# Kernel tuning notes

Measured on AMD Instinct MI355X. Metric: run time of the kernel, lower is better.

The kernel has to match this reference:

```python
import jax, jax.numpy as jnp
import numpy as np

N_NODES = 50000
N_EDGES = 800000
GEN_EPS = 1e-7
LN_EPS = 1e-5


def _mlp3_tanh(x, w0, b0, w1, b1, w2, b2):
    x = jnp.tanh(x @ w0.T + b0)
    x = jnp.tanh(x @ w1.T + b1)
    return jnp.tanh(x @ w2.T + b2)


def _gen_conv(x, src, dst, edge_attr, w0, b0, ln_w, ln_b, w1, b1):
    # GENConv(aggr='softmax', t=1): msg = relu(x_j + e) + eps
    msg = jax.nn.relu(x[src] + edge_attr) + GEN_EPS          # [E, 64]
    m = jax.ops.segment_max(msg, dst, num_segments=N_NODES)  # [N, 64]
    ex = jnp.exp(msg - m[dst])
    den = jax.ops.segment_sum(ex, dst, num_segments=N_NODES)
    alpha = ex / den[dst]                                    # scatter-softmax per dst
    agg = jax.ops.segment_sum(alpha * msg, dst, num_segments=N_NODES)
    h = x + agg                                              # x_r + aggregated messages
    # internal MLP: Linear(64->128), LayerNorm(128), ReLU, Linear(128->64)
    h = h @ w0.T + b0
    mu = jnp.mean(h, axis=-1, keepdims=True)
    var = jnp.mean((h - mu) ** 2, axis=-1, keepdims=True)
    h = ln_w * (h - mu) * jax.lax.rsqrt(var + LN_EPS) + ln_b
    h = jax.nn.relu(h)
    return h @ w1.T + b1


def setup_inputs() -> dict:
    key = jax.random.key(0)
    ks = jax.random.split(key, 32)
    s = 0.05
    d = {
        'node_features': jax.random.normal(ks[0], (N_NODES, 11), jnp.float32),
        'edge_features': jax.random.normal(ks[1], (N_EDGES, 3), jnp.float32),
        'edge_index': jax.random.randint(ks[2], (2, N_EDGES), 0, N_NODES, jnp.int32),
        'ne_w0': jax.random.normal(ks[3], (64, 11)) * s, 'ne_b0': jnp.zeros((64,)),
        'ne_w1': jax.random.normal(ks[4], (64, 64)) * s, 'ne_b1': jnp.zeros((64,)),
        'ne_w2': jax.random.normal(ks[5], (64, 64)) * s, 'ne_b2': jnp.zeros((64,)),
        'ee_w0': jax.random.normal(ks[6], (64, 3)) * s, 'ee_b0': jnp.zeros((64,)),
        'ee_w1': jax.random.normal(ks[7], (64, 64)) * s, 'ee_b1': jnp.zeros((64,)),
        'ee_w2': jax.random.normal(ks[8], (64, 64)) * s, 'ee_b2': jnp.zeros((64,)),
        'mp_w0': jax.random.normal(ks[9], (3, 128, 64)) * s,
        'mp_b0': jnp.zeros((3, 128)),
        'mp_ln_w': jnp.ones((3, 128)), 'mp_ln_b': jnp.zeros((3, 128)),
        'mp_w1': jax.random.normal(ks[10], (3, 64, 128)) * s,
        'mp_b1': jnp.zeros((3, 64)),
        'pi_w0': jax.random.normal(ks[11], (64, 64)) * s, 'pi_b0': jnp.zeros((64,)),
        'pi_w1': jax.random.normal(ks[12], (64, 64)) * s, 'pi_b1': jnp.zeros((64,)),
        'pi_w2': jax.random.normal(ks[13], (2, 64)) * s, 'pi_b2': jnp.zeros((2,)),
    }
    return {k: (v.astype(jnp.float32) if v.dtype != jnp.int32 else v) for k, v in d.items()}


def reference(node_features, edge_features, edge_index,
              ne_w0, ne_b0, ne_w1, ne_b1, ne_w2, ne_b2,
              ee_w0, ee_b0, ee_w1, ee_b1, ee_w2, ee_b2,
              mp_w0, mp_b0, mp_ln_w, mp_ln_b, mp_w1, mp_b1,
              pi_w0, pi_b0, pi_w1, pi_b1, pi_w2, pi_b2):
    src, dst = edge_index[0], edge_index[1]
    x = _mlp3_tanh(node_features, ne_w0, ne_b0, ne_w1, ne_b1, ne_w2, ne_b2)
    e = _mlp3_tanh(edge_features, ee_w0, ee_b0, ee_w1, ee_b1, ee_w2, ee_b2)
    for i in range(3):
        x = _gen_conv(x, src, dst, e, mp_w0[i], mp_b0[i], mp_ln_w[i], mp_ln_b[i], mp_w1[i], mp_b1[i])
    h = jnp.tanh(x @ pi_w0.T + pi_b0)
    h = jnp.tanh(h @ pi_w1.T + pi_b1)
    out = h @ pi_w2.T + pi_b2                 # [N, 2]
    # output.t().reshape(-1)[:n_turbines] == first column of out
    means = -30.0 + (out[:, 0] + 1.0) * 60.0 / 2.0
    return means
```

## Files before the change

kernel.cpp:

```cpp
#include <hip/hip_runtime.h>
#include <hip/hip_fp16.h>
#include <stdint.h>

#define N_NODES 50000
#define N_EDGES 800000

typedef unsigned short u16;
typedef unsigned int u32;
typedef __attribute__((ext_vector_type(8))) short short8;
typedef __attribute__((ext_vector_type(4))) float f32x4;
typedef __attribute__((ext_vector_type(4))) u32 u32x4;
typedef __attribute__((ext_vector_type(2))) u32 u32x2;

#define WAVE_SYNC() asm volatile("s_waitcnt lgkmcnt(0)" ::: "memory")

__device__ __forceinline__ float b2f(u16 v) {
    u32 u = ((u32)v) << 16; float f; __builtin_memcpy(&f, &u, 4); return f;
}
__device__ __forceinline__ u16 f2b(float f) {
    u32 u; __builtin_memcpy(&u, &f, 4);
    return (u16)((u + 0x8000u) >> 16);
}
__device__ __forceinline__ float lo2f(u32 p) {
    u32 u = p << 16; float f; __builtin_memcpy(&f, &u, 4); return f;
}
__device__ __forceinline__ float hi2f(u32 p) {
    u32 u = p & 0xffff0000u; float f; __builtin_memcpy(&f, &u, 4); return f;
}
__device__ __forceinline__ u32 pack2(float a, float b) {
    u32 ua, ub; __builtin_memcpy(&ua, &a, 4); __builtin_memcpy(&ub, &b, 4);
    return __builtin_amdgcn_perm(ub + 0x8000u, ua + 0x8000u, 0x07060302u);
}
__device__ __forceinline__ f32x4 mfma16(short8 a, short8 b, f32x4 c) {
    return __builtin_amdgcn_mfma_f32_16x16x32_bf16(a, b, c, 0, 0, 0);
}

__device__ __forceinline__ bool detect_bf(const void* nf) {
    u32 w = ((const u32*)nf)[threadIdx.x & 63];
    u32 lo = w & 0xffffu;
    int e = (int)((lo >> 7) & 0xff);
    int good = ((e >= 118 && e <= 132) || lo == 0) ? 1 : 0;
    unsigned long long b = __ballot(good != 0);
    return __popcll(b) >= 48;
}

#define TANH_TBL_N 256
__device__ __forceinline__ void load_tbl(const u32* __restrict__ g, u32* tbl) {
    int i = (int)threadIdx.x;
    if (i < TANH_TBL_N) tbl[i] = g[i];
    __syncthreads();
}
__device__ __forceinline__ float lut_tanh(const u32* __restrict__ tbl, float x) {
    float a = __builtin_fabsf(x);
    a = fminf(a, 7.96875f);
    int i = (int)(a * 32.f);
    u32 e = tbl[i];
    __half2 h2; __builtin_memcpy(&h2, &e, 4);
    float b = __half2float(__low2half(h2));
    float s = __half2float(__high2half(h2));
    return copysignf(fmaf(s, a, b), x);
}

enum : int {
    NE_B0 = 704,   NE_B1 = 4864,  NE_B2 = 9024,
    EE_B0 = 9280,  EE_B1 = 13440, EE_B2 = 17600,
    MP_B0 = 42240, LNW_O = 42624, LNB_O = 43008, MP_B1 = 67968,
    PI_B0 = 72256, PI_B1 = 76416, PI_W2 = 76480, PI_B2 = 76608,
    W_TOTAL = 76610
};

enum : int {
    FR_EE1 = 0, FR_EE2 = 4, FR_EE3 = 12, FR_NE1 = 20, FR_NE2 = 24, FR_NE3 = 32,
    FR_MP0 = 40, FR_MP1 = 88, FR_PI0 = 136, FR_PI1 = 144, FR_TOTAL = 152
};

#define OFF_W       ((size_t)0)
#define OFF_WB      ((size_t)0x61000)
#define OFF_TBL     ((size_t)0x88000)
#define OFF_XB0     ((size_t)0x90000)
#define OFF_XB1     ((size_t)0x700000)
#define OFF_H64B    ((size_t)0xE00000)
#define OFF_E       ((size_t)0x1500000)
#define OFF_ROWPTR  ((size_t)0x8300000)
#define OFF_CURSOR  ((size_t)0x8340000)
#define OFF_CNT     ((size_t)0x8380000)
#define OFF_PERM    ((size_t)0x83C0000)
#define OFF_SRCS    ((size_t)0x8700000)
#define OFF_BSUM    ((size_t)0x8A80000)

struct Ptrs24 { const void* p[24]; };

#define PREP_FRAG   (FR_TOTAL * 512)
#define PREP_BIAS   (PREP_FRAG + 1986)
#define PREP_LUT    (PREP_BIAS + TANH_TBL_N)
#define PREP_TOTAL  (PREP_LUT + N_NODES)

__global__ void prep_kernel(const void* nf, Ptrs24 ps, float* __restrict__ W,
                            u16* __restrict__ Wb, u32* __restrict__ gtbl,
                            int* __restrict__ cnts) {
    bool bf = detect_bf(nf);
    int t = blockIdx.x * blockDim.x + threadIdx.x;
    if (t < PREP_FRAG) {
        const int base[15] = {FR_EE1,FR_EE2,FR_EE3,FR_NE1,FR_NE2,FR_NE3,
                              FR_MP0,FR_MP0+16,FR_MP0+32, FR_MP1,FR_MP1+16,FR_MP1+32,
                              FR_PI0,FR_PI1,FR_TOTAL};
        const int psrc[14]  = {6,8,10, 0,2,4, 12,12,12, 16,16,16, 18,20};
        const int soff[14]  = {0,0,0, 0,0,0, 0,8192,16384, 0,8192,16384, 0,0};
        const int kreal[14] = {3,64,64, 11,64,64, 64,64,64, 128,128,128, 64,64};
        const int nn[14]    = {64,64,64, 64,64,64, 128,128,128, 64,64,64, 64,64};
        int f = t >> 9, r = t & 511, lane = r >> 3, j = r & 7;
        int l = 0;
        while (f >= base[l + 1]) l++;
        int lf = f - base[l];
        int NT = nn[l] >> 4;
        int kt = lf / NT, nt = lf % NT;
        int k = kt * 32 + (lane >> 4) * 8 + j;
        int n = nt * 16 + (lane & 15);
        float v = 0.f;
        if (k < kreal[l]) {
            long idx = (long)soff[l] + (long)n * kreal[l] + k;
            const void* p = ps.p[psrc[l]];
            v = bf ? b2f(((const u16*)p)[idx]) : ((const float*)p)[idx];
        }
        u32 u; __builtin_memcpy(&u, &v, 4);
        Wb[t] = (u16)((u + 0x7fffu + ((u >> 16) & 1u)) >> 16);
        return;
    }
    if (t < PREP_BIAS) {
        int t2 = t - PREP_FRAG;
        const int cnt[14]  = {64,64,64, 64,64,64, 384,384,384,192, 64,64,128,2};
        const int wdst[14] = {NE_B0,NE_B1,NE_B2, EE_B0,EE_B1,EE_B2,
                              MP_B0,LNW_O,LNB_O,MP_B1, PI_B0,PI_B1,PI_W2,PI_B2};
        const int sp[14]   = {1,3,5, 7,9,11, 13,14,15,17, 19,21,22,23};
        int sgi = 0, off = t2;
        while (off >= cnt[sgi]) { off -= cnt[sgi]; sgi++; }
        const void* p = ps.p[sp[sgi]];
        W[wdst[sgi] + off] = bf ? b2f(((const u16*)p)[off]) : ((const float*)p)[off];
        return;
    }
    if (t < PREP_LUT) {
        int i = t - PREP_BIAS;
        float x0 = i * 0.03125f, x1 = x0 + 0.03125f;
        float t0 = tanhf(x0), t1 = tanhf(x1);
        float s = (t1 - t0) * 32.f;
        float b = fmaf(-s, x0, t0);
        __half hs = __float2half(s), hb = __float2half(b);
        u16 us, ub;
        __builtin_memcpy(&us, &hs, 2); __builtin_memcpy(&ub, &hb, 2);
        gtbl[i] = (u32)ub | ((u32)us << 16);
        return;
    }
    if (t < PREP_TOTAL) cnts[t - PREP_LUT] = 0;
}


__global__ void hist_kernel(const int* __restrict__ dst, int* __restrict__ cnts) {
    int e = blockIdx.x * blockDim.x + threadIdx.x;
    if (e < N_EDGES) atomicAdd(&cnts[dst[e]], 1);
}

__global__ void scanA(const int* __restrict__ cnts, int* __restrict__ prow,
                      int* __restrict__ bsum) {
    __shared__ int wsum[16];
    int tid = threadIdx.x, lane = tid & 63, wid = tid >> 6;
    int i0 = blockIdx.x * 2048 + tid * 2;
    int v0 = 0, v1 = 0;
    if (i0 >= 1 && i0 <= N_NODES) v0 = (cnts[i0 - 1] + 1) & ~1;
    if (i0 + 1 <= N_NODES && i0 + 1 >= 1) v1 = (cnts[i0] + 1) & ~1;
    int v = v0 + v1;
#pragma unroll
    for (int off = 1; off < 64; off <<= 1) {
        int t = __shfl_up(v, off, 64);
        if (lane >= off) v += t;
    }
    if (lane == 63) wsum[wid] = v;
    __syncthreads();
    if (tid == 0) { int a = 0; for (int w = 0; w < 16; w++) { a += wsum[w]; wsum[w] = a; } }
    __syncthreads();
    int incl = v + (wid ? wsum[wid - 1] : 0);
    if (i0 <= N_NODES) prow[i0] = incl - v1;
    if (i0 + 1 <= N_NODES) prow[i0 + 1] = incl;
    if (tid == 1023) bsum[blockIdx.x] = incl;
}
__global__ void scanC(const int* __restrict__ bsum, const int* __restrict__ cnts,
                      int* __restrict__ prow, int* __restrict__ cursor,
                      int* __restrict__ srcs) {
    int i = blockIdx.x * 1024 + threadIdx.x;
    if (i > N_NODES) return;
    int nb = (int)(blockIdx.x >> 1);
    int add = 0;
    for (int b = 0; b < nb; b++) add += bsum[b];
    int v = prow[i] + add;
    prow[i] = v;
    if (i < N_NODES) {
        cursor[i] = v;
        int c = cnts[i];
        if (c & 1) srcs[v + c] = -1;
    }
}

__global__ void scatter_kernel(const int* __restrict__ dst, const int* __restrict__ src,
                               int* __restrict__ cursor, int* __restrict__ perm,
                               int* __restrict__ srcs) {
    int e = blockIdx.x * blockDim.x + threadIdx.x;
    if (e >= N_EDGES) return;
    int p = atomicAdd(&cursor[dst[e]], 1);
    perm[e] = p;
    srcs[p] = src[e];
}


template<int KT, int NT, int INSTR>
__device__ __forceinline__ void mfma_layer(const u32* ldsin, int lane,
        const short8* __restrict__ Wf, int basef, const float* __restrict__ bias, f32x4* acc) {
    int q = lane >> 4, mr = lane & 15;
#pragma unroll
    for (int nt = 0; nt < NT; nt++) acc[nt] = *(const f32x4*)(bias + nt * 16 + q * 4);
#pragma unroll
    for (int kt = 0; kt < KT; kt++) {
        short8 act = *(const short8*)(ldsin + mr * INSTR + kt * 16 + q * 4);
#pragma unroll
        for (int nt = 0; nt < NT; nt++)
            acc[nt] = mfma16(Wf[(basef + kt * NT + nt) * 64 + lane], act, acc[nt]);
    }
}

template<int KT, int NT>
__device__ __forceinline__ void mfma_layer_reg(const short8* act, int lane,
        const short8* __restrict__ Wf, int basef, const float* __restrict__ bias, f32x4* acc) {
    int q = lane >> 4;
#pragma unroll
    for (int nt = 0; nt < NT; nt++) acc[nt] = *(const f32x4*)(bias + nt * 16 + q * 4);
#pragma unroll
    for (int kt = 0; kt < KT; kt++)
#pragma unroll
        for (int nt = 0; nt < NT; nt++)
            acc[nt] = mfma16(Wf[(basef + kt * NT + nt) * 64 + lane], act[kt], acc[nt]);
}

template<int NT, int OUTSTR>
__device__ __forceinline__ void tanh_pack_lds(const f32x4* acc, u32* ldsout, int lane,
                                              const u32* __restrict__ tbl) {
    int q = lane >> 4, mr = lane & 15;
#pragma unroll
    for (int nt = 0; nt < NT; nt++) {
        f32x4 a = acc[nt];
        u32x2 pb;
        pb.x = pack2(lut_tanh(tbl, a[0]), lut_tanh(tbl, a[1]));
        pb.y = pack2(lut_tanh(tbl, a[2]), lut_tanh(tbl, a[3]));
        *(u32x2*)&ldsout[mr * OUTSTR + nt * 8 + q * 2] = pb;
    }
}

__device__ __forceinline__ void zero_stage(u32* B0, int lane) {
#pragma unroll
    for (int it = 0; it < 4; it++) {
        int f = lane + 64 * it;
        B0[(f >> 4) * 36 + (f & 15)] = 0;
    }
}


#define EDGE_SPLIT_BLOCKS (N_EDGES / 128)

__global__ __launch_bounds__(256) void edge_encoder(const void* nf, const void* ef,
        u32* __restrict__ ebuf, const int* __restrict__ perm, const float* __restrict__ W,
        const short8* __restrict__ Wf, const u32* __restrict__ gtbl, int part) {
    __shared__ u32 lds[4 * 1152];
    __shared__ u32 tbl[TANH_TBL_N];
    bool bf = detect_bf(nf);
    load_tbl(gtbl, tbl);
    int wv = threadIdx.x >> 6, lane = threadIdx.x & 63;
    u32* B0 = lds + wv * 1152;
    u32* B1 = B0 + 576;
    long ebase = ((long)blockIdx.x + (long)part * EDGE_SPLIT_BLOCKS) * 64 + wv * 16;
    zero_stage(B0, lane);
    if (lane < 16) {
        long e = ebase + lane;
        float i0, i1, i2;
        if (bf) { const u16* p = (const u16*)ef + e * 3; i0 = b2f(p[0]); i1 = b2f(p[1]); i2 = b2f(p[2]); }
        else    { const float* p = (const float*)ef + e * 3; i0 = p[0]; i1 = p[1]; i2 = p[2]; }
        u32* row = B0 + lane * 36;
        row[0] = pack2(i0, i1); row[1] = pack2(i2, 0.f);
    }
    WAVE_SYNC();
    f32x4 acc[4];
    mfma_layer<1, 4, 36>(B0, lane, Wf, FR_EE1, W + EE_B0, acc);
    tanh_pack_lds<4, 36>(acc, B1, lane, tbl);
    WAVE_SYNC();
    mfma_layer<2, 4, 36>(B1, lane, Wf, FR_EE2, W + EE_B1, acc);
    tanh_pack_lds<4, 36>(acc, B0, lane, tbl);
    WAVE_SYNC();
    mfma_layer<2, 4, 36>(B0, lane, Wf, FR_EE3, W + EE_B2, acc);
    tanh_pack_lds<4, 36>(acc, B1, lane, tbl);
    WAVE_SYNC();
    int ro = lane >> 2, cc = (lane & 3) * 8;
    long e = ebase + ro;
    long prowp = perm[e];
    u32x4 v0 = *(const u32x4*)&B1[ro * 36 + cc];
    u32x4 v1 = *(const u32x4*)&B1[ro * 36 + cc + 4];
    *(u32x4*)&ebuf[prowp * 32 + cc] = v0;
    *(u32x4*)&ebuf[prowp * 32 + cc + 4] = v1;
}

__global__ __launch_bounds__(256) void node_encoder(const void* nf,
        u16* __restrict__ xbf, const float* __restrict__ W,
        const short8* __restrict__ Wf, const u32* __restrict__ gtbl) {
    __shared__ u32 lds[4 * 1152];
    __shared__ u32 tbl[TANH_TBL_N];
    bool bf = detect_bf(nf);
    load_tbl(gtbl, tbl);
    int wv = threadIdx.x >> 6, lane = threadIdx.x & 63;
    int q = lane >> 4, mr = lane & 15;
    u32* B0 = lds + wv * 1152;
    u32* B1 = B0 + 576;
    long nbase = (long)blockIdx.x * 64 + wv * 16;
    zero_stage(B0, lane);
    if (lane < 16) {
        long n = nbase + lane;
        if (n < N_NODES) {
            float in[11];
#pragma unroll
            for (int j = 0; j < 11; j++)
                in[j] = bf ? b2f(((const u16*)nf)[n * 11 + j]) : ((const float*)nf)[n * 11 + j];
            u32* row = B0 + lane * 36;
#pragma unroll
            for (int d = 0; d < 5; d++) row[d] = pack2(in[2 * d], in[2 * d + 1]);
            row[5] = pack2(in[10], 0.f);
        }
    }
    WAVE_SYNC();
    f32x4 acc[4];
    mfma_layer<1, 4, 36>(B0, lane, Wf, FR_NE1, W + NE_B0, acc);
    tanh_pack_lds<4, 36>(acc, B1, lane, tbl);
    WAVE_SYNC();
    mfma_layer<2, 4, 36>(B1, lane, Wf, FR_NE2, W + NE_B1, acc);
    tanh_pack_lds<4, 36>(acc, B0, lane, tbl);
    WAVE_SYNC();
    mfma_layer<2, 4, 36>(B0, lane, Wf, FR_NE3, W + NE_B2, acc);
    long n = nbase + mr;
    if (n < N_NODES) {
#pragma unroll
        for (int nt = 0; nt < 4; nt++) {
            u32x2 pb;
            pb.x = pack2(lut_tanh(tbl, acc[nt][0]), lut_tanh(tbl, acc[nt][1]));
            pb.y = pack2(lut_tanh(tbl, acc[nt][2]), lut_tanh(tbl, acc[nt][3]));
            *(u32x2*)&xbf[n * 64 + nt * 16 + q * 4] = pb;
        }
    }
}

template<int R>
__global__ __launch_bounds__(256) void aggregate_kernel(
        const u32* __restrict__ xbf32, const u32* __restrict__ ebuf32,
        const int* __restrict__ srcs, const int* __restrict__ prow,
        u32* __restrict__ h64bf32) {
    __shared__ int ldsW[4][64];
    int wv = threadIdx.x >> 6;
    int wid = (int)((blockIdx.x * 256 + threadIdx.x) >> 6);
    int lane = (int)(threadIdx.x & 63);
    int n0 = __builtin_amdgcn_readfirstlane(wid) * 2;
    if (n0 >= N_NODES) return;
    int qt = lane >> 4, h16 = lane & 15;
    int rl = n0 + (lane < 2 ? lane : 2);
    int rv = prow[rl];
    int kb0 = __shfl(rv, 0, 64);
    int kb1 = __shfl(rv, 1, 64);
    int kb2 = __shfl(rv, 2, 64);
    float an[2][4], ad[2][4];
#pragma unroll
    for (int j = 0; j < 2; j++)
#pragma unroll
        for (int f = 0; f < 4; f++) { an[j][f] = 0.f; ad[j][f] = 0.f; }
    for (int wb = kb0; wb < kb2; wb += 64) {
        ldsW[wv][lane] = srcs[wb + lane];
        WAVE_SYNC();
        int we = wb + 64;
        int hi0 = kb1 < we ? kb1 : we;
        int lo1 = kb1 > wb ? kb1 : wb;
        int hi1 = kb2 < we ? kb2 : we;
#pragma unroll 2
        for (int k = wb; k < hi0; k += 4) {
            int e = k + qt;
            int eoc = (e < hi0) ? e : (hi0 - 1);
            int s = ldsW[wv][eoc - wb];
            u32x2 ev = *(const u32x2*)&ebuf32[(size_t)eoc * 32 + 2 * h16];
            u32x2 xv = *(const u32x2*)&xbf32[(size_t)(s > 0 ? s : 0) * 32 + 2 * h16];
            float vf = (e < hi0 && s >= 0) ? 1.f : 0.f;
            float m0 = fmaxf(lo2f(xv.x) + lo2f(ev.x), 0.f) + 1e-7f;
            float m1 = fmaxf(hi2f(xv.x) + hi2f(ev.x), 0.f) + 1e-7f;
            float m2 = fmaxf(lo2f(xv.y) + lo2f(ev.y), 0.f) + 1e-7f;
            float m3 = fmaxf(hi2f(xv.y) + hi2f(ev.y), 0.f) + 1e-7f;
            float w0 = __expf(m0) * vf, w1 = __expf(m1) * vf;
            float w2 = __expf(m2) * vf, w3 = __expf(m3) * vf;
            an[0][0] = fmaf(w0, m0, an[0][0]); ad[0][0] += w0;
            an[0][1] = fmaf(w1, m1, an[0][1]); ad[0][1] += w1;
            an[0][2] = fmaf(w2, m2, an[0][2]); ad[0][2] += w2;
            an[0][3] = fmaf(w3, m3, an[0][3]); ad[0][3] += w3;
        }
#pragma unroll 2
        for (int k = lo1; k < hi1; k += 4) {
            int e = k + qt;
            int eoc = (e < hi1) ? e : (hi1 - 1);
            int s = ldsW[wv][eoc - wb];
            u32x2 ev = *(const u32x2*)&ebuf32[(size_t)eoc * 32 + 2 * h16];
            u32x2 xv = *(const u32x2*)&xbf32[(size_t)(s > 0 ? s : 0) * 32 + 2 * h16];
            float vf = (e < hi1 && s >= 0) ? 1.f : 0.f;
            float m0 = fmaxf(lo2f(xv.x) + lo2f(ev.x), 0.f) + 1e-7f;
            float m1 = fmaxf(hi2f(xv.x) + hi2f(ev.x), 0.f) + 1e-7f;
            float m2 = fmaxf(lo2f(xv.y) + lo2f(ev.y), 0.f) + 1e-7f;
            float m3 = fmaxf(hi2f(xv.y) + hi2f(ev.y), 0.f) + 1e-7f;
            float w0 = __expf(m0) * vf, w1 = __expf(m1) * vf;
            float w2 = __expf(m2) * vf, w3 = __expf(m3) * vf;
            an[1][0] = fmaf(w0, m0, an[1][0]); ad[1][0] += w0;
            an[1][1] = fmaf(w1, m1, an[1][1]); ad[1][1] += w1;
            an[1][2] = fmaf(w2, m2, an[1][2]); ad[1][2] += w2;
            an[1][3] = fmaf(w3, m3, an[1][3]); ad[1][3] += w3;
        }
        WAVE_SYNC();
    }
#pragma unroll
    for (int j = 0; j < 2; j++) {
#pragma unroll
        for (int f = 0; f < 4; f++) {
            an[j][f] += __shfl_xor(an[j][f], 16, 64);
            an[j][f] += __shfl_xor(an[j][f], 32, 64);
            ad[j][f] += __shfl_xor(ad[j][f], 16, 64);
            ad[j][f] += __shfl_xor(ad[j][f], 32, 64);
        }
        if (qt == 0) {
            float a0 = (ad[j][0] > 0.f) ? __fdividef(an[j][0], ad[j][0]) : 0.f;
            float a1 = (ad[j][1] > 0.f) ? __fdividef(an[j][1], ad[j][1]) : 0.f;
            float a2 = (ad[j][2] > 0.f) ? __fdividef(an[j][2], ad[j][2]) : 0.f;
            float a3 = (ad[j][3] > 0.f) ? __fdividef(an[j][3], ad[j][3]) : 0.f;
            u32x2 xr = *(const u32x2*)&xbf32[(size_t)(n0 + j) * 32 + 2 * h16];
            u32x2 o;
            o.x = pack2(lo2f(xr.x) + a0, hi2f(xr.x) + a1);
            o.y = pack2(lo2f(xr.y) + a2, hi2f(xr.y) + a3);
            *(u32x2*)&h64bf32[(size_t)(n0 + j) * 32 + 2 * h16] = o;
        }
    }
}

__global__ __launch_bounds__(256) void mlp_fused(const u16* __restrict__ h64bf,
        u16* __restrict__ xbf,
        const float* __restrict__ W, const short8* __restrict__ Wf, int r) {
    __shared__ u32 lds[4 * 1088];
    int wv = threadIdx.x >> 6, lane = threadIdx.x & 63;
    int q = lane >> 4, mr = lane & 15;
    u32* bufY = lds + wv * 1088;
    long nbase = (long)blockIdx.x * 64 + wv * 16;
    long row = nbase + mr;
    long rc = (row < N_NODES) ? row : (N_NODES - 1);
    short8 act[2];
#pragma unroll
    for (int kt = 0; kt < 2; kt++)
        act[kt] = *(const short8*)&h64bf[rc * 64 + kt * 32 + q * 8];
    f32x4 acc[8];
    mfma_layer_reg<2, 8>(act, lane, Wf, FR_MP0 + r * 16, W + MP_B0 + r * 128, acc);
    float s = 0.f, sq = 0.f;
#pragma unroll
    for (int nt = 0; nt < 8; nt++)
#pragma unroll
        for (int rr = 0; rr < 4; rr++) { float v = acc[nt][rr]; s += v; sq = fmaf(v, v, sq); }
    s += __shfl_xor(s, 16, 64);  s += __shfl_xor(s, 32, 64);
    sq += __shfl_xor(sq, 16, 64); sq += __shfl_xor(sq, 32, 64);
    float mu = s * (1.f / 128.f);
    float var = sq * (1.f / 128.f) - mu * mu;
    float inv = rsqrtf(var + 1e-5f);
    const float* LW = W + LNW_O + r * 128;
    const float* LB = W + LNB_O + r * 128;
#pragma unroll
    for (int nt = 0; nt < 8; nt++) {
        f32x4 lw = *(const f32x4*)(LW + nt * 16 + q * 4);
        f32x4 lb = *(const f32x4*)(LB + nt * 16 + q * 4);
        float u0 = fmaxf(fmaf((acc[nt][0] - mu) * inv, lw[0], lb[0]), 0.f);
        float u1 = fmaxf(fmaf((acc[nt][1] - mu) * inv, lw[1], lb[1]), 0.f);
        float u2 = fmaxf(fmaf((acc[nt][2] - mu) * inv, lw[2], lb[2]), 0.f);
        float u3 = fmaxf(fmaf((acc[nt][3] - mu) * inv, lw[3], lb[3]), 0.f);
        u32x2 pb; pb.x = pack2(u0, u1); pb.y = pack2(u2, u3);
        *(u32x2*)&bufY[mr * 68 + nt * 8 + q * 2] = pb;
    }
    WAVE_SYNC();
    f32x4 acc2[4];
    mfma_layer<4, 4, 68>(bufY, lane, Wf, FR_MP1 + r * 16, W + MP_B1 + r * 64, acc2);
    if (row < N_NODES) {
#pragma unroll
        for (int nt = 0; nt < 4; nt++) {
            f32x4 v = acc2[nt];
            u32x2 pb; pb.x = pack2(v[0], v[1]); pb.y = pack2(v[2], v[3]);
            *(u32x2*)&xbf[row * 64 + nt * 16 + q * 4] = pb;
        }
    }
}

__global__ __launch_bounds__(256) void policy_head(const void* nf,
        const u16* __restrict__ xbf, void* out, const float* __restrict__ W,
        const short8* __restrict__ Wf, const u32* __restrict__ gtbl) {
    __shared__ u32 lds[4 * 576];
    __shared__ u32 tbl[TANH_TBL_N];
    bool bf = detect_bf(nf);
    load_tbl(gtbl, tbl);
    int wv = threadIdx.x >> 6, lane = threadIdx.x & 63;
    int q = lane >> 4, mr = lane & 15;
    u32* bufY = lds + wv * 576;
    long nbase = (long)blockIdx.x * 64 + wv * 16;
    long row = nbase + mr;
    long rc = (row < N_NODES) ? row : (N_NODES - 1);
    short8 act[2];
#pragma unroll
    for (int kt = 0; kt < 2; kt++)
        act[kt] = *(const short8*)&xbf[rc * 64 + kt * 32 + q * 8];
    f32x4 acc[4];
    mfma_layer_reg<2, 4>(act, lane, Wf, FR_PI0, W + PI_B0, acc);
    tanh_pack_lds<4, 36>(acc, bufY, lane, tbl);
    WAVE_SYNC();
    mfma_layer<2, 4, 36>(bufY, lane, Wf, FR_PI1, W + PI_B1, acc);
    float o = 0.f;
#pragma unroll
    for (int nt = 0; nt < 4; nt++) {
        f32x4 w2 = *(const f32x4*)(W + PI_W2 + nt * 16 + q * 4);
#pragma unroll
        for (int rr = 0; rr < 4; rr++) o = fmaf(lut_tanh(tbl, acc[nt][rr]), w2[rr], o);
    }
    o += __shfl_xor(o, 16, 64);
    o += __shfl_xor(o, 32, 64);
    if (lane < 16 && row < N_NODES) {
        float means = 30.f * (o + W[PI_B2]);
        if (bf) ((u16*)out)[row] = f2b(means);
        else    ((float*)out)[row] = means;
    }
}

extern "C" void kernel_launch(void* const* d_in, const int* in_sizes, int n_in,
                              void* d_out, int out_size, void* d_ws, size_t ws_size,
                              hipStream_t stream) {
    char* ws = (char*)d_ws;
    float* W      = (float*)(ws + OFF_W);
    u16*   Wb     = (u16*)(ws + OFF_WB);
    const short8* Wf = (const short8*)(ws + OFF_WB);
    u32*   gtbl   = (u32*)(ws + OFF_TBL);
    u16*   xb0    = (u16*)(ws + OFF_XB0);
    u16*   xb1    = (u16*)(ws + OFF_XB1);
    u16*   h64bf  = (u16*)(ws + OFF_H64B);
    u32*   h64b32 = (u32*)(ws + OFF_H64B);
    u32*   ebuf32 = (u32*)(ws + OFF_E);
    int*   prow   = (int*)(ws + OFF_ROWPTR);
    int*   cursor = (int*)(ws + OFF_CURSOR);
    int*   cnts   = (int*)(ws + OFF_CNT);
    int*   perm   = (int*)(ws + OFF_PERM);
    int*   srcs   = (int*)(ws + OFF_SRCS);
    int*   bsum   = (int*)(ws + OFF_BSUM);

    const void* nf  = d_in[0];
    const int* ei   = (const int*)d_in[2];
    const int* srcv = ei;
    const int* dstv = ei + N_EDGES;

    Ptrs24 ps;
    for (int k = 0; k < 24; k++) ps.p[k] = d_in[3 + k];
    prep_kernel<<<(PREP_TOTAL + 255) / 256, 256, 0, stream>>>(nf, ps, W, Wb, gtbl, cnts);

    hist_kernel<<<(N_EDGES + 255) / 256, 256, 0, stream>>>(dstv, cnts);
    scanA<<<25, 1024, 0, stream>>>(cnts, prow, bsum);
    scanC<<<(N_NODES + 1024) / 1024, 1024, 0, stream>>>(bsum, cnts, prow, cursor, srcs);
    scatter_kernel<<<(N_EDGES + 255) / 256, 256, 0, stream>>>(dstv, srcv, cursor, perm, srcs);

    node_encoder<<<(N_NODES + 63) / 64, 256, 0, stream>>>(nf, xb0, W, Wf, gtbl);
    edge_encoder<<<EDGE_SPLIT_BLOCKS, 256, 0, stream>>>(nf, d_in[1], ebuf32, perm, W, Wf, gtbl, 0);
    edge_encoder<<<EDGE_SPLIT_BLOCKS, 256, 0, stream>>>(nf, d_in[1], ebuf32, perm, W, Wf, gtbl, 1);

    u16* xbc = xb0; u16* xbn = xb1;
    const int aggBlocks = (N_NODES / 2 * 64) / 256;
    aggregate_kernel<0><<<aggBlocks, 256, 0, stream>>>((const u32*)xbc, ebuf32, srcs, prow, h64b32);
    mlp_fused<<<(N_NODES + 63) / 64, 256, 0, stream>>>(h64bf, xbn, W, Wf, 0);
    { u16* tb = xbc; xbc = xbn; xbn = tb; }
    aggregate_kernel<1><<<aggBlocks, 256, 0, stream>>>((const u32*)xbc, ebuf32, srcs, prow, h64b32);
    mlp_fused<<<(N_NODES + 63) / 64, 256, 0, stream>>>(h64bf, xbn, W, Wf, 1);
    { u16* tb = xbc; xbc = xbn; xbn = tb; }
    aggregate_kernel<2><<<aggBlocks, 256, 0, stream>>>((const u32*)xbc, ebuf32, srcs, prow, h64b32);
    mlp_fused<<<(N_NODES + 63) / 64, 256, 0, stream>>>(h64bf, xbn, W, Wf, 2);
    { u16* tb = xbc; xbc = xbn; xbn = tb; }

    policy_head<<<(N_NODES + 63) / 64, 256, 0, stream>>>(nf, xbc, d_out, W, Wf, gtbl);
}
```

Before: 422.9 us.

## Build CSR with per-segment counts and ranks for edge-order-stable layout

```diff
diff --git a/kernel.cpp b/kernel.cpp
--- a/kernel.cpp
+++ b/kernel.cpp
@@ -4,6 +4,8 @@
 
 #define N_NODES 50000
 #define N_EDGES 800000
+#define SEG 16
+#define M_ITEMS (SEG * N_NODES)
 
 typedef unsigned short u16;
 typedef unsigned int u32;
@@ -81,23 +83,24 @@
 #define OFF_XB1     ((size_t)0x700000)
 #define OFF_H64B    ((size_t)0xE00000)
 #define OFF_E       ((size_t)0x1500000)
-#define OFF_ROWPTR  ((size_t)0x8300000)
-#define OFF_CURSOR  ((size_t)0x8340000)
-#define OFF_CNT     ((size_t)0x8380000)
-#define OFF_PERM    ((size_t)0x83C0000)
-#define OFF_SRCS    ((size_t)0x8700000)
-#define OFF_BSUM    ((size_t)0x8A80000)
+#define OFF_PRA     ((size_t)0x8300000)
+#define OFF_CNT16   ((size_t)0x8700000)
+#define OFF_CNTT    ((size_t)0x8B00000)
+#define OFF_PERM    ((size_t)0x8C00000)
+#define OFF_RANK    ((size_t)0x9000000)
+#define OFF_SRCS    ((size_t)0x9400000)
+#define OFF_BSUM    ((size_t)0x9780000)
 
 struct Ptrs24 { const void* p[24]; };
 
 #define PREP_FRAG   (FR_TOTAL * 512)
 #define PREP_BIAS   (PREP_FRAG + 1986)
 #define PREP_LUT    (PREP_BIAS + TANH_TBL_N)
-#define PREP_TOTAL  (PREP_LUT + N_NODES)
+#define PREP_TOTAL  (PREP_LUT + M_ITEMS)
 
 __global__ void prep_kernel(const void* nf, Ptrs24 ps, float* __restrict__ W,
                             u16* __restrict__ Wb, u32* __restrict__ gtbl,
-                            int* __restrict__ cnts) {
+                            int* __restrict__ cnt16) {
     bool bf = detect_bf(nf);
     int t = blockIdx.x * blockDim.x + threadIdx.x;
     if (t < PREP_FRAG) {
@@ -150,23 +153,35 @@
         gtbl[i] = (u32)ub | ((u32)us << 16);
         return;
     }
-    if (t < PREP_TOTAL) cnts[t - PREP_LUT] = 0;
-}
-
-
-__global__ void hist_kernel(const int* __restrict__ dst, int* __restrict__ cnts) {
+    if (t < PREP_TOTAL) cnt16[t - PREP_LUT] = 0;
+}
+
+
+__global__ void hist_kernel(const int* __restrict__ dst, int* __restrict__ cnt16,
+                            int* __restrict__ rank) {
     int e = blockIdx.x * blockDim.x + threadIdx.x;
-    if (e < N_EDGES) atomicAdd(&cnts[dst[e]], 1);
-}
-
-__global__ void scanA(const int* __restrict__ cnts, int* __restrict__ prow,
+    if (e >= N_EDGES) return;
+    int g = e >> 16;
+    rank[e] = atomicAdd(&cnt16[dst[e] * SEG + g], 1);
+}
+
+__global__ void padfix_kernel(int* __restrict__ cnt16, int* __restrict__ cntTot) {
+    int d = blockIdx.x * blockDim.x + threadIdx.x;
+    if (d >= N_NODES) return;
+    int C = 0;
+#pragma unroll
+    for (int g = 0; g < SEG; g++) C += cnt16[d * SEG + g];
+    cntTot[d] = C;
+    if (C & 1) cnt16[d * SEG + SEG - 1] += 1;
+}
+
+__global__ void scanA(const int* __restrict__ cnt16, int* __restrict__ pra,
                       int* __restrict__ bsum) {
     __shared__ int wsum[16];
     int tid = threadIdx.x, lane = tid & 63, wid = tid >> 6;
     int i0 = blockIdx.x * 2048 + tid * 2;
-    int v0 = 0, v1 = 0;
-    if (i0 >= 1 && i0 <= N_NODES) v0 = (cnts[i0 - 1] + 1) & ~1;
-    if (i0 + 1 <= N_NODES && i0 + 1 >= 1) v1 = (cnts[i0] + 1) & ~1;
+    int v0 = (i0 >= 1 && i0 <= M_ITEMS) ? cnt16[i0 - 1] : 0;
+    int v1 = (i0 + 1 <= M_ITEMS) ? cnt16[i0] : 0;
     int v = v0 + v1;
 #pragma unroll
     for (int off = 1; off < 64; off <<= 1) {
@@ -178,33 +193,48 @@
     if (tid == 0) { int a = 0; for (int w = 0; w < 16; w++) { a += wsum[w]; wsum[w] = a; } }
     __syncthreads();
     int incl = v + (wid ? wsum[wid - 1] : 0);
-    if (i0 <= N_NODES) prow[i0] = incl - v1;
-    if (i0 + 1 <= N_NODES) prow[i0 + 1] = incl;
+    if (i0 <= M_ITEMS) pra[i0] = incl - v1;
+    if (i0 + 1 <= M_ITEMS) pra[i0 + 1] = incl;
     if (tid == 1023) bsum[blockIdx.x] = incl;
 }
-__global__ void scanC(const int* __restrict__ bsum, const int* __restrict__ cnts,
-                      int* __restrict__ prow, int* __restrict__ cursor,
-                      int* __restrict__ srcs) {
+
+__global__ void scanB(int* __restrict__ bsum, int nb) {
+    int lane = (int)threadIdx.x;
+    int carry = 0;
+    for (int base = 0; base < nb; base += 64) {
+        int v = (base + lane < nb) ? bsum[base + lane] : 0;
+#pragma unroll
+        for (int off = 1; off < 64; off <<= 1) {
+            int t = __shfl_up(v, off, 64);
+            if (lane >= off) v += t;
+        }
+        int tot = __shfl(v, 63, 64);
+        if (base + lane < nb) bsum[base + lane] = v + carry;
+        carry += tot;
+    }
+}
+
+__global__ void scanC(const int* __restrict__ bsum, const int* __restrict__ cntTot,
+                      int* __restrict__ pra, int* __restrict__ srcs) {
     int i = blockIdx.x * 1024 + threadIdx.x;
-    if (i > N_NODES) return;
-    int nb = (int)(blockIdx.x >> 1);
-    int add = 0;
-    for (int b = 0; b < nb; b++) add += bsum[b];
-    int v = prow[i] + add;
-    prow[i] = v;
-    if (i < N_NODES) {
-        cursor[i] = v;
-        int c = cnts[i];
-        if (c & 1) srcs[v + c] = -1;
+    if (i > M_ITEMS) return;
+    int b = i >> 11;
+    int v = pra[i] + (b ? bsum[b - 1] : 0);
+    pra[i] = v;
+    if (i < M_ITEMS && (i & (SEG - 1)) == 0) {
+        int d = i / SEG;
+        int C = cntTot[d];
+        if (C & 1) srcs[v + C] = -1;
     }
 }
 
 __global__ void scatter_kernel(const int* __restrict__ dst, const int* __restrict__ src,
-                               int* __restrict__ cursor, int* __restrict__ perm,
-                               int* __restrict__ srcs) {
+                               const int* __restrict__ rank, const int* __restrict__ pra,
+                               int* __restrict__ perm, int* __restrict__ srcs) {
     int e = blockIdx.x * blockDim.x + threadIdx.x;
     if (e >= N_EDGES) return;
-    int p = atomicAdd(&cursor[dst[e]], 1);
+    int g = e >> 16;
+    int p = pra[dst[e] * SEG + g] + rank[e];
     perm[e] = p;
     srcs[p] = src[e];
 }
@@ -350,20 +380,21 @@
     }
 }
 
+#define AGG_HALF_WAVES (N_NODES / 4)
 template<int R>
 __global__ __launch_bounds__(256) void aggregate_kernel(
         const u32* __restrict__ xbf32, const u32* __restrict__ ebuf32,
-        const int* __restrict__ srcs, const int* __restrict__ prow,
-        u32* __restrict__ h64bf32) {
+        const int* __restrict__ srcs, const int* __restrict__ pra,
+        u32* __restrict__ h64bf32, int part) {
     __shared__ int ldsW[4][64];
     int wv = threadIdx.x >> 6;
-    int wid = (int)((blockIdx.x * 256 + threadIdx.x) >> 6);
+    int wid = (int)((blockIdx.x * 256 + threadIdx.x) >> 6) + part * AGG_HALF_WAVES;
     int lane = (int)(threadIdx.x & 63);
     int n0 = __builtin_amdgcn_readfirstlane(wid) * 2;
     if (n0 >= N_NODES) return;
     int qt = lane >> 4, h16 = lane & 15;
     int rl = n0 + (lane < 2 ? lane : 2);
-    int rv = prow[rl];
+    int rv = pra[rl * SEG];
     int kb0 = __shfl(rv, 0, 64);
     int kb1 = __shfl(rv, 1, 64);
     int kb2 = __shfl(rv, 2, 64);
@@ -545,10 +576,11 @@
     u16*   h64bf  = (u16*)(ws + OFF_H64B);
     u32*   h64b32 = (u32*)(ws + OFF_H64B);
     u32*   ebuf32 = (u32*)(ws + OFF_E);
-    int*   prow   = (int*)(ws + OFF_ROWPTR);
-    int*   cursor = (int*)(ws + OFF_CURSOR);
-    int*   cnts   = (int*)(ws + OFF_CNT);
+    int*   pra    = (int*)(ws + OFF_PRA);
+    int*   cnt16  = (int*)(ws + OFF_CNT16);
+    int*   cntTot = (int*)(ws + OFF_CNTT);
     int*   perm   = (int*)(ws + OFF_PERM);
+    int*   rank   = (int*)(ws + OFF_RANK);
     int*   srcs   = (int*)(ws + OFF_SRCS);
     int*   bsum   = (int*)(ws + OFF_BSUM);
 
@@ -559,26 +591,32 @@
 
     Ptrs24 ps;
     for (int k = 0; k < 24; k++) ps.p[k] = d_in[3 + k];
-    prep_kernel<<<(PREP_TOTAL + 255) / 256, 256, 0, stream>>>(nf, ps, W, Wb, gtbl, cnts);
-
-    hist_kernel<<<(N_EDGES + 255) / 256, 256, 0, stream>>>(dstv, cnts);
-    scanA<<<25, 1024, 0, stream>>>(cnts, prow, bsum);
-    scanC<<<(N_NODES + 1024) / 1024, 1024, 0, stream>>>(bsum, cnts, prow, cursor, srcs);
-    scatter_kernel<<<(N_EDGES + 255) / 256, 256, 0, stream>>>(dstv, srcv, cursor, perm, srcs);
+    prep_kernel<<<(PREP_TOTAL + 255) / 256, 256, 0, stream>>>(nf, ps, W, Wb, gtbl, cnt16);
+
+    hist_kernel<<<(N_EDGES + 255) / 256, 256, 0, stream>>>(dstv, cnt16, rank);
+    padfix_kernel<<<(N_NODES + 255) / 256, 256, 0, stream>>>(cnt16, cntTot);
+    const int scanABlocks = (M_ITEMS + 1 + 2047) / 2048;
+    scanA<<<scanABlocks, 1024, 0, stream>>>(cnt16, pra, bsum);
+    scanB<<<1, 64, 0, stream>>>(bsum, scanABlocks);
+    scanC<<<(M_ITEMS + 1024) / 1024, 1024, 0, stream>>>(bsum, cntTot, pra, srcs);
+    scatter_kernel<<<(N_EDGES + 255) / 256, 256, 0, stream>>>(dstv, srcv, rank, pra, perm, srcs);
 
     node_encoder<<<(N_NODES + 63) / 64, 256, 0, stream>>>(nf, xb0, W, Wf, gtbl);
     edge_encoder<<<EDGE_SPLIT_BLOCKS, 256, 0, stream>>>(nf, d_in[1], ebuf32, perm, W, Wf, gtbl, 0);
     edge_encoder<<<EDGE_SPLIT_BLOCKS, 256, 0, stream>>>(nf, d_in[1], ebuf32, perm, W, Wf, gtbl, 1);
 
     u16* xbc = xb0; u16* xbn = xb1;
-    const int aggBlocks = (N_NODES / 2 * 64) / 256;
-    aggregate_kernel<0><<<aggBlocks, 256, 0, stream>>>((const u32*)xbc, ebuf32, srcs, prow, h64b32);
+    const int aggHalfBlocks = AGG_HALF_WAVES / 4;
+    aggregate_kernel<0><<<aggHalfBlocks, 256, 0, stream>>>((const u32*)xbc, ebuf32, srcs, pra, h64b32, 0);
+    aggregate_kernel<0><<<aggHalfBlocks, 256, 0, stream>>>((const u32*)xbc, ebuf32, srcs, pra, h64b32, 1);
     mlp_fused<<<(N_NODES + 63) / 64, 256, 0, stream>>>(h64bf, xbn, W, Wf, 0);
     { u16* tb = xbc; xbc = xbn; xbn = tb; }
-    aggregate_kernel<1><<<aggBlocks, 256, 0, stream>>>((const u32*)xbc, ebuf32, srcs, prow, h64b32);
+    aggregate_kernel<1><<<aggHalfBlocks, 256, 0, stream>>>((const u32*)xbc, ebuf32, srcs, pra, h64b32, 0);
+    aggregate_kernel<1><<<aggHalfBlocks, 256, 0, stream>>>((const u32*)xbc, ebuf32, srcs, pra, h64b32, 1);
     mlp_fused<<<(N_NODES + 63) / 64, 256, 0, stream>>>(h64bf, xbn, W, Wf, 1);
     { u16* tb = xbc; xbc = xbn; xbn = tb; }
-    aggregate_kernel<2><<<aggBlocks, 256, 0, stream>>>((const u32*)xbc, ebuf32, srcs, prow, h64b32);
+    aggregate_kernel<2><<<aggHalfBlocks, 256, 0, stream>>>((const u32*)xbc, ebuf32, srcs, pra, h64b32, 0);
+    aggregate_kernel<2><<<aggHalfBlocks, 256, 0, stream>>>((const u32*)xbc, ebuf32, srcs, pra, h64b32, 1);
     mlp_fused<<<(N_NODES + 63) / 64, 256, 0, stream>>>(h64bf, xbn, W, Wf, 2);
     { u16* tb = xbc; xbc = xbn; xbn = tb; }
 
```

Result: no change. 417.3 us (-1.3%).
